# Performance work log

Hardware: AMD Instinct MI355X
Metric: run time of the kernel (lower is better)

The kernel has to match this reference:

```python
import jax, jax.numpy as jnp
import numpy as np

D_MODEL = 512
NUM_HEADS = 8
D_K = D_MODEL // NUM_HEADS
SCALE = float(np.sqrt(D_K))


def setup_inputs() -> dict:
    key = jax.random.key(0)
    ks = jax.random.split(key, 11)
    B, S, D = 2, 4096, D_MODEL
    std = 1.0 / np.sqrt(D)
    return {
        "query": jax.random.normal(ks[0], (B, S, D), jnp.float32),
        "key": jax.random.normal(ks[1], (B, S, D), jnp.float32),
        "value": jax.random.normal(ks[2], (B, S, D), jnp.float32),
        "w_q": jax.random.normal(ks[3], (D, D), jnp.float32) * std,
        "b_q": jax.random.normal(ks[4], (D,), jnp.float32) * std,
        "w_k": jax.random.normal(ks[5], (D, D), jnp.float32) * std,
        "b_k": jax.random.normal(ks[6], (D,), jnp.float32) * std,
        "w_v": jax.random.normal(ks[7], (D, D), jnp.float32) * std,
        "b_v": jax.random.normal(ks[8], (D,), jnp.float32) * std,
        "w_o": jax.random.normal(ks[9], (D, D), jnp.float32) * std,
        "b_o": jax.random.normal(ks[10], (D,), jnp.float32) * std,
    }


def reference(query, key, value, w_q, b_q, w_k, b_k, w_v, b_v, w_o, b_o):
    B, S, D = query.shape
    H, Dk = NUM_HEADS, D_K
    # Linear projections (torch Linear: x @ W^T + b), split into heads -> [B,H,S,Dk]
    Q = (query @ w_q.T + b_q).reshape(B, S, H, Dk).transpose(0, 2, 1, 3)
    K = (key @ w_k.T + b_k).reshape(B, S, H, Dk).transpose(0, 2, 1, 3)
    V = (value @ w_v.T + b_v).reshape(B, S, H, Dk).transpose(0, 2, 1, 3)
    # [B,H,S,S] attention scores — intentionally materialized like the original
    scores = jnp.einsum("bhqd,bhkd->bhqk", Q, K) / SCALE
    attn = jax.nn.softmax(scores, axis=-1)  # dropout rate 0 in eval baseline
    attended = jnp.einsum("bhqk,bhkd->bhqd", attn, V)
    attended = attended.transpose(0, 2, 1, 3).reshape(B, S, D)
    return attended @ w_o.T + b_o
```

## Files before the change

### kernel.cpp

```cpp
#include <hip/hip_runtime.h>
#include <math.h>

#define D_MODEL 512
#define NHEADS 8
#define DK 64
#define BATCH 2
#define SEQ 4096
#define NIT 32
#define ATTN_SCALE 0.18033688011112043f

typedef _Float16 half8 __attribute__((ext_vector_type(8)));
typedef _Float16 half4 __attribute__((ext_vector_type(4)));
typedef __fp16 pkhalf2 __attribute__((ext_vector_type(2)));
typedef float f32x4 __attribute__((ext_vector_type(4)));
typedef float f32x16 __attribute__((ext_vector_type(16)));

union Pk8 { _Float16 h[8]; uint4 u; };
union Pk4 { _Float16 h[4]; uint2 u; };
union Pkz { pkhalf2 h2[2]; uint2 u; };
union Un4 { uint2 u; _Float16 h[4]; };
union PFu { unsigned int u[4]; half8 h8; };

#if __has_builtin(__builtin_amdgcn_exp2f)
#define EXP2F __builtin_amdgcn_exp2f
#else
#define EXP2F exp2f
#endif

#define MFMA16(a, b, c) __builtin_amdgcn_mfma_f32_16x16x32_f16((a), (b), (c), 0, 0, 0)
#define MFMA32(a, b, c) __builtin_amdgcn_mfma_f32_32x32x16_f16((a), (b), (c), 0, 0, 0)

#define PLSWAP(x, y) asm volatile("v_permlane32_swap_b32 %0, %1" : "+v"(x), "+v"(y))

__device__ __forceinline__ unsigned int cvtpk(float a, float b) {
    union { pkhalf2 h; unsigned int u; } u_;
    u_.h = __builtin_amdgcn_cvt_pkrtz(a, b);
    return u_.u;
}

__device__ __forceinline__ void gload_lds16(const _Float16* g, _Float16* l) {
    __builtin_amdgcn_global_load_lds(
        (const __attribute__((address_space(1))) void*)g,
        (__attribute__((address_space(3))) void*)l, 16, 0, 0);
}

#define ABLK 4096
#define WBLK 256
__global__ __launch_bounds__(256)
void prep(const float* __restrict__ aq, const float* __restrict__ ak,
          const float* __restrict__ av,
          const float* __restrict__ wq, const float* __restrict__ wk,
          const float* __restrict__ wv, const float* __restrict__ wo,
          _Float16* __restrict__ dq, _Float16* __restrict__ dk,
          _Float16* __restrict__ dv,
          _Float16* __restrict__ hq, _Float16* __restrict__ hk,
          _Float16* __restrict__ hv, _Float16* __restrict__ ho) {
    int gid = blockIdx.x;
    const float* src;
    _Float16* hi;
    if (gid < 3 * ABLK) {
        const int w = gid / ABLK;
        gid -= w * ABLK;
        src = w == 0 ? aq : (w == 1 ? ak : av);
        hi  = w == 0 ? dq : (w == 1 ? dk : dv);
    } else {
        int g = gid - 3 * ABLK;
        const int w = g / WBLK;
        gid = g - w * WBLK;
        src = w == 0 ? wq : (w == 1 ? wk : (w == 2 ? wv : wo));
        hi  = w == 0 ? hq : (w == 1 ? hk : (w == 2 ? hv : ho));
    }
    const int i = (gid * 256 + threadIdx.x) * 4;
    float4 v = *(const float4*)(src + i);
    Pkz h;
    h.h2[0] = __builtin_amdgcn_cvt_pkrtz(v.x, v.y);
    h.h2[1] = __builtin_amdgcn_cvt_pkrtz(v.z, v.w);
    *(uint2*)(hi + i) = h.u;
}

__global__ __launch_bounds__(256)
void gemm_qkv(const _Float16* __restrict__ Aq, const _Float16* __restrict__ Ak,
              const _Float16* __restrict__ Av,
              const _Float16* __restrict__ Whq, const _Float16* __restrict__ Whk,
              const _Float16* __restrict__ Whv,
              const float* __restrict__ bq, const float* __restrict__ bk,
              const float* __restrict__ bv,
              _Float16* __restrict__ Qf, _Float16* __restrict__ Kf,
              _Float16* __restrict__ Vtf) {
    const int z = blockIdx.z;
    const _Float16* A    = z == 0 ? Aq  : (z == 1 ? Ak  : Av);
    const _Float16* Wh   = z == 0 ? Whq : (z == 1 ? Whk : Whv);
    const float*    bias = z == 0 ? bq  : (z == 1 ? bk  : bv);

    __shared__ __align__(16) _Float16 sA[2][128 * 64];
    __shared__ __align__(16) _Float16 sW[2][128 * 64];

    const int t    = threadIdx.x;
    const int lane = t & 63, wave = t >> 6;
    const int col  = lane & 15, quad = lane >> 4;
    const int wm   = (wave & 1) * 64, wn = (wave >> 1) * 64;
    const int m0   = blockIdx.y * 128, n0 = blockIdx.x * 128;

    const int subrow = lane >> 3;
    const int schunk = ((lane & 7) ^ subrow) * 8;

    #define STAGE_AW(K0, BUF)                                                        \
        do {                                                                          \
            _Pragma("unroll")                                                         \
            for (int j = 0; j < 4; ++j) {                                             \
                const int rw = wave * 32 + j * 8;                                     \
                gload_lds16(A  + (size_t)(m0 + rw + subrow) * 512 + (K0) + schunk,    \
                            &sA[BUF][rw * 64]);                                       \
                gload_lds16(Wh + (size_t)(n0 + rw + subrow) * 512 + (K0) + schunk,    \
                            &sW[BUF][rw * 64]);                                       \
            }                                                                         \
        } while (0)

    f32x4 acc[4][4] = {};

    STAGE_AW(0, 0);
    for (int ck = 0; ck < 8; ++ck) {
        const int cur = ck & 1;
        __syncthreads();
        if (ck + 1 < 8) STAGE_AW((ck + 1) * 64, cur ^ 1);

        #pragma unroll
        for (int kc = 0; kc < 2; ++kc) {
            const int pos = ((kc * 4 + quad) ^ (col & 7)) * 8;
            half8 af[4], wf[4];
            #pragma unroll
            for (int mt = 0; mt < 4; ++mt)
                af[mt] = *(const half8*)&sA[cur][(wm + mt * 16 + col) * 64 + pos];
            #pragma unroll
            for (int nt = 0; nt < 4; ++nt)
                wf[nt] = *(const half8*)&sW[cur][(wn + nt * 16 + col) * 64 + pos];
            #pragma unroll
            for (int mt = 0; mt < 4; ++mt)
                #pragma unroll
                for (int nt = 0; nt < 4; ++nt)
                    acc[mt][nt] = MFMA16(af[mt], wf[nt], acc[mt][nt]);
        }
    }

    float bv4[4];
    #pragma unroll
    for (int nt = 0; nt < 4; ++nt) bv4[nt] = bias[n0 + wn + nt * 16 + col];

    if (z < 2) {
        _Float16* Out = z == 0 ? Qf : Kf;
        const float alpha = z == 0 ? ATTN_SCALE : 1.0f;
        #pragma unroll
        for (int mt = 0; mt < 4; ++mt) {
            const int m = m0 + wm + mt * 16 + quad * 4;
            #pragma unroll
            for (int nt = 0; nt < 4; ++nt) {
                const int n = n0 + wn + nt * 16 + col;
                #pragma unroll
                for (int r = 0; r < 4; ++r)
                    Out[(size_t)(m + r) * 512 + n] = (_Float16)((acc[mt][nt][r] + bv4[nt]) * alpha);
            }
        }
    } else {
        #pragma unroll
        for (int mt = 0; mt < 4; ++mt) {
            const int m = m0 + wm + mt * 16 + quad * 4;
            const int b = m >> 12, s = m & (SEQ - 1);
            #pragma unroll
            for (int nt = 0; nt < 4; ++nt) {
                const int n = n0 + wn + nt * 16 + col;
                const int hh = n >> 6, d = n & (DK - 1);
                Pk4 p;
                #pragma unroll
                for (int r = 0; r < 4; ++r)
                    p.h[r] = (_Float16)(acc[mt][nt][r] + bv4[nt]);
                *(uint2*)&Vtf[((size_t)((b * NHEADS + hh) * DK + d)) * SEQ + s] = p.u;
            }
        }
    }
}

__global__ __launch_bounds__(256, 2)
void attn_mfma(const _Float16* __restrict__ Qf, const _Float16* __restrict__ Kf,
               const _Float16* __restrict__ Vtf,
               _Float16* __restrict__ Op0, _Float16* __restrict__ Op1,
               float2* __restrict__ Ml) {
    __shared__ __align__(16) _Float16 sK[2][64 * 64];
    __shared__ __align__(16) _Float16 sV[2][64 * 64];

    const int t    = threadIdx.x;
    const int lane = t & 63;
    const int wave = t >> 6;
    const int l31  = lane & 31;
    const int g    = lane >> 5;

    const int strm = blockIdx.x;
    const int h  = strm & (NHEADS - 1);
    const int z  = strm >> 3;
    const int b  = z >> 1;
    const int sp = z & 1;
    const int q0 = blockIdx.y * 256;
    const int kBase = sp * (SEQ / 2);

    const size_t rowBase = (size_t)b * SEQ;
    const size_t vBase   = ((size_t)(b * NHEADS + h)) * DK * SEQ;

    const int subrow = lane >> 3;
    const int schunk = ((lane & 7) ^ subrow) * 8;
    const _Float16* kP[2];
    const _Float16* vP[2];
    #pragma unroll
    for (int j = 0; j < 2; ++j) {
        const int rw = wave * 16 + j * 8;
        kP[j] = Kf + (rowBase + kBase + rw + subrow) * 512 + h * 64 + schunk;
        vP[j] = Vtf + vBase + (size_t)(rw + subrow) * SEQ + kBase + schunk;
        gload_lds16(kP[j], &sK[0][rw * 64]);
        gload_lds16(vP[j], &sV[0][rw * 64]);
        kP[j] += 64 * 512;
        vP[j] += 64;
    }

    half8 qf[2][4];
    #pragma unroll
    for (int qt = 0; qt < 2; ++qt)
        #pragma unroll
        for (int kc = 0; kc < 4; ++kc)
            qf[qt][kc] = *(const half8*)(Qf +
                (rowBase + q0 + wave * 64 + qt * 32 + l31) * 512 +
                h * 64 + kc * 16 + g * 8);

    const int rs = l31 & 7;

    const half8 ones = {1, 1, 1, 1, 1, 1, 1, 1};

    float m_r = 0.0f;
    f32x16 nbv = {};
    f32x16 of[2][2] = {};
    f32x16 ofl[2] = {};

    for (int itp = 0; itp < NIT; itp += 2) {
        #pragma unroll
        for (int cur = 0; cur < 2; ++cur) {
            const int it = itp + cur;
            __syncthreads();
            if (it + 1 < NIT) {
                #pragma unroll
                for (int j = 0; j < 2; ++j) {
                    const int rw = wave * 16 + j * 8;
                    gload_lds16(kP[j], &sK[cur ^ 1][rw * 64]);
                    gload_lds16(vP[j], &sV[cur ^ 1][rw * 64]);
                    kP[j] += 64 * 512;
                    vP[j] += 64;
                }
            }

            #pragma unroll
            for (int kt = 0; kt < 2; ++kt) {
                f32x16 sf0, sf1;
                __builtin_amdgcn_s_setprio(1);
                #pragma unroll
                for (int kc = 0; kc < 4; ++kc) {
                    const int pos = ((kc * 2 + g) ^ rs) * 8;
                    half8 kf = *(const half8*)&sK[cur][(kt * 32 + l31) * 64 + pos];
                    sf0 = MFMA32(kf, qf[0][kc], kc == 0 ? nbv : sf0);
                    sf1 = MFMA32(kf, qf[1][kc], kc == 0 ? nbv : sf1);
                }
                __builtin_amdgcn_s_setprio(0);

                #pragma unroll
                for (int j2 = 0; j2 < 16; ++j2) {
                    sf0[j2] = EXP2F(sf0[j2]);
                    sf1[j2] = EXP2F(sf1[j2]);
                }

                PFu pf0[2], pf1[2];
                #define MKPF(P, PF)                                                  \
                    do {                                                             \
                        unsigned int x1 = cvtpk(P[0], P[1]),  x2 = cvtpk(P[2], P[3]);\
                        unsigned int y1 = cvtpk(P[4], P[5]),  y2 = cvtpk(P[6], P[7]);\
                        PLSWAP(x1, y1); PLSWAP(x2, y2);                              \
                        PF[0].u[0] = x1; PF[0].u[1] = x2;                            \
                        PF[0].u[2] = y1; PF[0].u[3] = y2;                            \
                        unsigned int a1 = cvtpk(P[8], P[9]),  a2 = cvtpk(P[10], P[11]);\
                        unsigned int b1 = cvtpk(P[12], P[13]), b2 = cvtpk(P[14], P[15]);\
                        PLSWAP(a1, b1); PLSWAP(a2, b2);                              \
                        PF[1].u[0] = a1; PF[1].u[1] = a2;                            \
                        PF[1].u[2] = b1; PF[1].u[3] = b2;                            \
                    } while (0)
                MKPF(sf0, pf0);
                MKPF(sf1, pf1);
                #undef MKPF

                __builtin_amdgcn_s_setprio(1);
                #pragma unroll
                for (int ks2 = 0; ks2 < 2; ++ks2) {
                    const int ks = kt * 2 + ks2;
                    const int pos = ((ks * 2 + g) ^ rs) * 8;
                    half8 v0 = *(const half8*)&sV[cur][l31 * 64 + pos];
                    half8 v1 = *(const half8*)&sV[cur][(32 + l31) * 64 + pos];
                    of[0][0] = MFMA32(v0, pf0[ks2].h8, of[0][0]);
                    of[0][1] = MFMA32(v1, pf0[ks2].h8, of[0][1]);
                    of[1][0] = MFMA32(v0, pf1[ks2].h8, of[1][0]);
                    of[1][1] = MFMA32(v1, pf1[ks2].h8, of[1][1]);
                    ofl[0] = MFMA32(ones, pf0[ks2].h8, ofl[0]);
                    ofl[1] = MFMA32(ones, pf1[ks2].h8, ofl[1]);
                }
                __builtin_amdgcn_s_setprio(0);
            }

            if (__any(fmaxf(ofl[0][0], ofl[1][0]) > 1048576.0f)) {
                const float al = 0.0009765625f;
                #pragma unroll
                for (int qt = 0; qt < 2; ++qt) {
                    #pragma unroll
                    for (int j2 = 0; j2 < 16; ++j2) {
                        of[qt][0][j2] *= al;
                        of[qt][1][j2] *= al;
                        ofl[qt][j2]   *= al;
                    }
                }
                m_r += 10.0f;
                #pragma unroll
                for (int j2 = 0; j2 < 16; ++j2) nbv[j2] = -m_r;
            }
        }
    }

    _Float16* Opx = sp ? Op1 : Op0;
    #pragma unroll
    for (int qt = 0; qt < 2; ++qt) {
        const float l = ofl[qt][0];
        const float inv = 1.0f / l;
        const int q = q0 + wave * 64 + qt * 32 + l31;
        const size_t R = rowBase + q;
        #pragma unroll
        for (int dt = 0; dt < 2; ++dt) {
            #pragma unroll
            for (int m4 = 0; m4 < 4; ++m4) {
                const int d0 = dt * 32 + 8 * m4 + 4 * g;
                Pkz z2;
                z2.h2[0] = __builtin_amdgcn_cvt_pkrtz(of[qt][dt][4 * m4 + 0] * inv,
                                                      of[qt][dt][4 * m4 + 1] * inv);
                z2.h2[1] = __builtin_amdgcn_cvt_pkrtz(of[qt][dt][4 * m4 + 2] * inv,
                                                      of[qt][dt][4 * m4 + 3] * inv);
                *(uint2*)(Opx + R * 512 + h * 64 + d0) = z2.u;
            }
        }
        if (lane < 32)
            Ml[(size_t)(sp * BATCH * SEQ) * NHEADS + R * NHEADS + h] = make_float2(m_r, l);
    }
}

__global__ __launch_bounds__(256)
void attn_merge(const _Float16* __restrict__ Op0, const _Float16* __restrict__ Op1,
                const float2* __restrict__ Ml, _Float16* __restrict__ Oh) {
    const int i4 = (blockIdx.x * 256 + threadIdx.x) * 4;
    const int R = i4 >> 9;
    const int c = i4 & 511;
    const int h = c >> 6;

    const float2 ml1 = Ml[(size_t)R * NHEADS + h];
    const float2 ml2 = Ml[(size_t)(BATCH * SEQ) * NHEADS + (size_t)R * NHEADS + h];
    const float m = fmaxf(ml1.x, ml2.x);
    float w1 = EXP2F(ml1.x - m) * ml1.y;
    float w2 = EXP2F(ml2.x - m) * ml2.y;
    const float inv = 1.0f / (w1 + w2);
    w1 *= inv; w2 *= inv;

    Un4 a, bb;
    a.u  = *(const uint2*)(Op0 + (size_t)R * 512 + c);
    bb.u = *(const uint2*)(Op1 + (size_t)R * 512 + c);

    Pkz hh;
    hh.h2[0] = __builtin_amdgcn_cvt_pkrtz(w1 * (float)a.h[0] + w2 * (float)bb.h[0],
                                          w1 * (float)a.h[1] + w2 * (float)bb.h[1]);
    hh.h2[1] = __builtin_amdgcn_cvt_pkrtz(w1 * (float)a.h[2] + w2 * (float)bb.h[2],
                                          w1 * (float)a.h[3] + w2 * (float)bb.h[3]);
    *(uint2*)(Oh + (size_t)R * 512 + c) = hh.u;
}

__global__ __launch_bounds__(256)
void gemm_out(const _Float16* __restrict__ Ah, const _Float16* __restrict__ Wh,
              const float* __restrict__ bias, float* __restrict__ C) {
    __shared__ __align__(16) _Float16 sAh[2][128 * 64];
    __shared__ __align__(16) _Float16 sWh[2][64 * 64];

    const int t    = threadIdx.x;
    const int lane = t & 63, wave = t >> 6;
    const int col  = lane & 15, quad = lane >> 4;
    const int wm   = (wave & 1) * 64, wn = (wave >> 1) * 32;
    const int m0   = blockIdx.y * 128, n0 = blockIdx.x * 64;

    const int subrow = lane >> 3;
    const int schunk = ((lane & 7) ^ subrow) * 8;

    #define STAGE_OUT(K0, BUF)                                                       \
        do {                                                                          \
            _Pragma("unroll")                                                         \
            for (int j = 0; j < 4; ++j) {                                             \
                const int rw = wave * 32 + j * 8;                                     \
                gload_lds16(Ah + (size_t)(m0 + rw + subrow) * 512 + (K0) + schunk,    \
                            &sAh[BUF][rw * 64]);                                      \
            }                                                                         \
            _Pragma("unroll")                                                         \
            for (int j = 0; j < 2; ++j) {                                             \
                const int rw = wave * 16 + j * 8;                                     \
                gload_lds16(Wh + (size_t)(n0 + rw + subrow) * 512 + (K0) + schunk,    \
                            &sWh[BUF][rw * 64]);                                      \
            }                                                                         \
        } while (0)

    f32x4 acc[4][2] = {};

    STAGE_OUT(0, 0);
    for (int ck = 0; ck < 8; ++ck) {
        const int cur = ck & 1;
        __syncthreads();
        if (ck + 1 < 8) STAGE_OUT((ck + 1) * 64, cur ^ 1);

        #pragma unroll
        for (int kc = 0; kc < 2; ++kc) {
            const int pos = ((kc * 4 + quad) ^ (col & 7)) * 8;
            half8 ahf[4], whf[2];
            #pragma unroll
            for (int mt = 0; mt < 4; ++mt)
                ahf[mt] = *(const half8*)&sAh[cur][(wm + mt * 16 + col) * 64 + pos];
            #pragma unroll
            for (int nt = 0; nt < 2; ++nt)
                whf[nt] = *(const half8*)&sWh[cur][(wn + nt * 16 + col) * 64 + pos];
            #pragma unroll
            for (int mt = 0; mt < 4; ++mt)
                #pragma unroll
                for (int nt = 0; nt < 2; ++nt)
                    acc[mt][nt] = MFMA16(ahf[mt], whf[nt], acc[mt][nt]);
        }
    }

    float bv2[2];
    #pragma unroll
    for (int nt = 0; nt < 2; ++nt) bv2[nt] = bias[n0 + wn + nt * 16 + col];

    #pragma unroll
    for (int mt = 0; mt < 4; ++mt) {
        const int m = m0 + wm + mt * 16 + quad * 4;
        #pragma unroll
        for (int nt = 0; nt < 2; ++nt) {
            const int n = n0 + wn + nt * 16 + col;
            #pragma unroll
            for (int r = 0; r < 4; ++r)
                C[(size_t)(m + r) * 512 + n] = acc[mt][nt][r] + bv2[nt];
        }
    }
}

extern "C" void kernel_launch(void* const* d_in, const int* in_sizes, int n_in,
                              void* d_out, int out_size, void* d_ws, size_t ws_size,
                              hipStream_t stream) {
    const float* query = (const float*)d_in[0];
    const float* key   = (const float*)d_in[1];
    const float* value = (const float*)d_in[2];
    const float* w_q   = (const float*)d_in[3];
    const float* b_q   = (const float*)d_in[4];
    const float* w_k   = (const float*)d_in[5];
    const float* b_k   = (const float*)d_in[6];
    const float* w_v   = (const float*)d_in[7];
    const float* b_v   = (const float*)d_in[8];
    const float* w_o   = (const float*)d_in[9];
    const float* b_o   = (const float*)d_in[10];
    float* out = (float*)d_out;

    const int WN = D_MODEL * D_MODEL;
    const size_t plane = (size_t)BATCH * SEQ * D_MODEL;

    _Float16* base = (_Float16*)d_ws;
    _Float16* Aq16 = base;
    _Float16* Ak16 = Aq16 + plane;
    _Float16* Av16 = Ak16 + plane;
    _Float16* whq  = Av16 + plane;
    _Float16* whk  = whq + WN;
    _Float16* whv  = whk + WN;
    _Float16* who  = whv + WN;
    _Float16* Qf   = who + WN;
    _Float16* Kf   = Qf + plane;
    _Float16* Vtf  = Kf + plane;
    _Float16* Op1  = Vtf + plane;
    float2*   Ml   = (float2*)(Op1 + plane);
    _Float16* Oh   = Aq16;
    _Float16* Op0  = Av16;

    dim3 blk(256);

    hipLaunchKernelGGL(prep, dim3(3 * ABLK + 4 * WBLK), blk, 0, stream,
                       query, key, value, w_q, w_k, w_v, w_o,
                       Aq16, Ak16, Av16, whq, whk, whv, who);

    hipLaunchKernelGGL(gemm_qkv, dim3(D_MODEL / 128, BATCH * SEQ / 128, 3), blk, 0, stream,
                       Aq16, Ak16, Av16,
                       whq, whk, whv,
                       b_q, b_k, b_v, Qf, Kf, Vtf);

    hipLaunchKernelGGL(attn_mfma, dim3(NHEADS * BATCH * 2, SEQ / 256), blk, 0, stream,
                       Qf, Kf, Vtf, Op0, Op1, Ml);

    hipLaunchKernelGGL(attn_merge, dim3(BATCH * SEQ * D_MODEL / 4 / 256), blk, 0, stream,
                       Op0, Op1, Ml, Oh);

    hipLaunchKernelGGL(gemm_out, dim3(D_MODEL / 64, BATCH * SEQ / 128), blk, 0, stream,
                       Oh, who, b_o, out);
}
```

Before: 239.3 us.

## Split attention keys four ways and compute row sums on VALU

```diff
diff --git a/kernel.cpp b/kernel.cpp
--- a/kernel.cpp
+++ b/kernel.cpp
@@ -6,7 +6,8 @@
 #define DK 64
 #define BATCH 2
 #define SEQ 4096
-#define NIT 32
+#define NSPLIT 4
+#define NIT 16
 #define ATTN_SCALE 0.18033688011112043f
 
 typedef _Float16 half8 __attribute__((ext_vector_type(8)));
@@ -179,10 +180,11 @@
     }
 }
 
-__global__ __launch_bounds__(256, 2)
+__global__ __launch_bounds__(256, 4)
 void attn_mfma(const _Float16* __restrict__ Qf, const _Float16* __restrict__ Kf,
                const _Float16* __restrict__ Vtf,
                _Float16* __restrict__ Op0, _Float16* __restrict__ Op1,
+               _Float16* __restrict__ Op2, _Float16* __restrict__ Op3,
                float2* __restrict__ Ml) {
     __shared__ __align__(16) _Float16 sK[2][64 * 64];
     __shared__ __align__(16) _Float16 sV[2][64 * 64];
@@ -196,10 +198,10 @@
     const int strm = blockIdx.x;
     const int h  = strm & (NHEADS - 1);
     const int z  = strm >> 3;
-    const int b  = z >> 1;
-    const int sp = z & 1;
+    const int b  = z >> 2;
+    const int sp = z & 3;
     const int q0 = blockIdx.y * 256;
-    const int kBase = sp * (SEQ / 2);
+    const int kBase = sp * (SEQ / NSPLIT);
 
     const size_t rowBase = (size_t)b * SEQ;
     const size_t vBase   = ((size_t)(b * NHEADS + h)) * DK * SEQ;
@@ -230,12 +232,10 @@
 
     const int rs = l31 & 7;
 
-    const half8 ones = {1, 1, 1, 1, 1, 1, 1, 1};
-
     float m_r = 0.0f;
     f32x16 nbv = {};
+    float l_r[2] = { 0.0f, 0.0f };
     f32x16 of[2][2] = {};
-    f32x16 ofl[2] = {};
 
     for (int itp = 0; itp < NIT; itp += 2) {
         #pragma unroll
@@ -266,11 +266,14 @@
                 }
                 __builtin_amdgcn_s_setprio(0);
 
+                float lrs0 = 0.0f, lrs1 = 0.0f;
                 #pragma unroll
                 for (int j2 = 0; j2 < 16; ++j2) {
-                    sf0[j2] = EXP2F(sf0[j2]);
-                    sf1[j2] = EXP2F(sf1[j2]);
+                    sf0[j2] = EXP2F(sf0[j2]);  lrs0 += sf0[j2];
+                    sf1[j2] = EXP2F(sf1[j2]);  lrs1 += sf1[j2];
                 }
+                l_r[0] += lrs0;
+                l_r[1] += lrs1;
 
                 PFu pf0[2], pf1[2];
                 #define MKPF(P, PF)                                                  \
@@ -301,21 +304,19 @@
                     of[0][1] = MFMA32(v1, pf0[ks2].h8, of[0][1]);
                     of[1][0] = MFMA32(v0, pf1[ks2].h8, of[1][0]);
                     of[1][1] = MFMA32(v1, pf1[ks2].h8, of[1][1]);
-                    ofl[0] = MFMA32(ones, pf0[ks2].h8, ofl[0]);
-                    ofl[1] = MFMA32(ones, pf1[ks2].h8, ofl[1]);
                 }
                 __builtin_amdgcn_s_setprio(0);
             }
 
-            if (__any(fmaxf(ofl[0][0], ofl[1][0]) > 1048576.0f)) {
+            if (__any(fmaxf(l_r[0], l_r[1]) > 1048576.0f)) {
                 const float al = 0.0009765625f;
                 #pragma unroll
                 for (int qt = 0; qt < 2; ++qt) {
+                    l_r[qt] *= al;
                     #pragma unroll
                     for (int j2 = 0; j2 < 16; ++j2) {
                         of[qt][0][j2] *= al;
                         of[qt][1][j2] *= al;
-                        ofl[qt][j2]   *= al;
                     }
                 }
                 m_r += 10.0f;
@@ -325,10 +326,10 @@
         }
     }
 
-    _Float16* Opx = sp ? Op1 : Op0;
+    _Float16* Opx = sp == 0 ? Op0 : (sp == 1 ? Op1 : (sp == 2 ? Op2 : Op3));
     #pragma unroll
     for (int qt = 0; qt < 2; ++qt) {
-        const float l = ofl[qt][0];
+        const float l = l_r[qt] + __shfl_xor(l_r[qt], 32);
         const float inv = 1.0f / l;
         const int q = q0 + wave * 64 + qt * 32 + l31;
         const size_t R = rowBase + q;
@@ -346,35 +347,47 @@
             }
         }
         if (lane < 32)
-            Ml[(size_t)(sp * BATCH * SEQ) * NHEADS + R * NHEADS + h] = make_float2(m_r, l);
+            Ml[((size_t)sp * BATCH * SEQ + R) * NHEADS + h] = make_float2(m_r, l);
     }
 }
 
 __global__ __launch_bounds__(256)
 void attn_merge(const _Float16* __restrict__ Op0, const _Float16* __restrict__ Op1,
+                const _Float16* __restrict__ Op2, const _Float16* __restrict__ Op3,
                 const float2* __restrict__ Ml, _Float16* __restrict__ Oh) {
     const int i4 = (blockIdx.x * 256 + threadIdx.x) * 4;
     const int R = i4 >> 9;
     const int c = i4 & 511;
     const int h = c >> 6;
 
-    const float2 ml1 = Ml[(size_t)R * NHEADS + h];
-    const float2 ml2 = Ml[(size_t)(BATCH * SEQ) * NHEADS + (size_t)R * NHEADS + h];
-    const float m = fmaxf(ml1.x, ml2.x);
+    const size_t mlStride = (size_t)BATCH * SEQ * NHEADS;
+    const size_t mlIdx = (size_t)R * NHEADS + h;
+    float2 ml0 = Ml[mlIdx];
+    float2 ml1 = Ml[mlStride + mlIdx];
+    float2 ml2 = Ml[2 * mlStride + mlIdx];
+    float2 ml3 = Ml[3 * mlStride + mlIdx];
+    const float m = fmaxf(fmaxf(ml0.x, ml1.x), fmaxf(ml2.x, ml3.x));
+    float w0 = EXP2F(ml0.x - m) * ml0.y;
     float w1 = EXP2F(ml1.x - m) * ml1.y;
     float w2 = EXP2F(ml2.x - m) * ml2.y;
-    const float inv = 1.0f / (w1 + w2);
-    w1 *= inv; w2 *= inv;
-
-    Un4 a, bb;
+    float w3 = EXP2F(ml3.x - m) * ml3.y;
+    const float inv = 1.0f / (w0 + w1 + w2 + w3);
+    w0 *= inv; w1 *= inv; w2 *= inv; w3 *= inv;
+
+    Un4 a, bb, cc, dd;
     a.u  = *(const uint2*)(Op0 + (size_t)R * 512 + c);
     bb.u = *(const uint2*)(Op1 + (size_t)R * 512 + c);
+    cc.u = *(const uint2*)(Op2 + (size_t)R * 512 + c);
+    dd.u = *(const uint2*)(Op3 + (size_t)R * 512 + c);
+
+    float o0 = w0 * (float)a.h[0] + w1 * (float)bb.h[0] + w2 * (float)cc.h[0] + w3 * (float)dd.h[0];
+    float o1 = w0 * (float)a.h[1] + w1 * (float)bb.h[1] + w2 * (float)cc.h[1] + w3 * (float)dd.h[1];
+    float o2 = w0 * (float)a.h[2] + w1 * (float)bb.h[2] + w2 * (float)cc.h[2] + w3 * (float)dd.h[2];
+    float o3 = w0 * (float)a.h[3] + w1 * (float)bb.h[3] + w2 * (float)cc.h[3] + w3 * (float)dd.h[3];
 
     Pkz hh;
-    hh.h2[0] = __builtin_amdgcn_cvt_pkrtz(w1 * (float)a.h[0] + w2 * (float)bb.h[0],
-                                          w1 * (float)a.h[1] + w2 * (float)bb.h[1]);
-    hh.h2[1] = __builtin_amdgcn_cvt_pkrtz(w1 * (float)a.h[2] + w2 * (float)bb.h[2],
-                                          w1 * (float)a.h[3] + w2 * (float)bb.h[3]);
+    hh.h2[0] = __builtin_amdgcn_cvt_pkrtz(o0, o1);
+    hh.h2[1] = __builtin_amdgcn_cvt_pkrtz(o2, o3);
     *(uint2*)(Oh + (size_t)R * 512 + c) = hh.u;
 }
 
@@ -486,6 +499,8 @@
     float2*   Ml   = (float2*)(Op1 + plane);
     _Float16* Oh   = Aq16;
     _Float16* Op0  = Av16;
+    _Float16* Op2  = Ak16;
+    _Float16* Op3  = Aq16;
 
     dim3 blk(256);
 
@@ -498,11 +513,11 @@
                        whq, whk, whv,
                        b_q, b_k, b_v, Qf, Kf, Vtf);
 
-    hipLaunchKernelGGL(attn_mfma, dim3(NHEADS * BATCH * 2, SEQ / 256), blk, 0, stream,
-                       Qf, Kf, Vtf, Op0, Op1, Ml);
+    hipLaunchKernelGGL(attn_mfma, dim3(NHEADS * BATCH * NSPLIT, SEQ / 256), blk, 0, stream,
+                       Qf, Kf, Vtf, Op0, Op1, Op2, Op3, Ml);
 
     hipLaunchKernelGGL(attn_merge, dim3(BATCH * SEQ * D_MODEL / 4 / 256), blk, 0, stream,
-                       Op0, Op1, Ml, Oh);
+                       Op0, Op1, Op2, Op3, Ml, Oh);
 
     hipLaunchKernelGGL(gemm_out, dim3(D_MODEL / 64, BATCH * SEQ / 128), blk, 0, stream,
                        Oh, who, b_o, out);
```

After: 880.5 us. +268.0%, slower.

## Fuse activation fp16 conversion into QKV GEMM and compute softmax sums on VALU

Applied to the files above, without the earlier changes.

```diff
diff --git a/kernel.cpp b/kernel.cpp
--- a/kernel.cpp
+++ b/kernel.cpp
@@ -6,6 +6,7 @@
 #define DK 64
 #define BATCH 2
 #define SEQ 4096
+#define NSPLIT 2
 #define NIT 32
 #define ATTN_SCALE 0.18033688011112043f
 
@@ -44,32 +45,17 @@
         (__attribute__((address_space(3))) void*)l, 16, 0, 0);
 }
 
-#define ABLK 4096
 #define WBLK 256
 __global__ __launch_bounds__(256)
-void prep(const float* __restrict__ aq, const float* __restrict__ ak,
-          const float* __restrict__ av,
-          const float* __restrict__ wq, const float* __restrict__ wk,
+void prep(const float* __restrict__ wq, const float* __restrict__ wk,
           const float* __restrict__ wv, const float* __restrict__ wo,
-          _Float16* __restrict__ dq, _Float16* __restrict__ dk,
-          _Float16* __restrict__ dv,
           _Float16* __restrict__ hq, _Float16* __restrict__ hk,
           _Float16* __restrict__ hv, _Float16* __restrict__ ho) {
     int gid = blockIdx.x;
-    const float* src;
-    _Float16* hi;
-    if (gid < 3 * ABLK) {
-        const int w = gid / ABLK;
-        gid -= w * ABLK;
-        src = w == 0 ? aq : (w == 1 ? ak : av);
-        hi  = w == 0 ? dq : (w == 1 ? dk : dv);
-    } else {
-        int g = gid - 3 * ABLK;
-        const int w = g / WBLK;
-        gid = g - w * WBLK;
-        src = w == 0 ? wq : (w == 1 ? wk : (w == 2 ? wv : wo));
-        hi  = w == 0 ? hq : (w == 1 ? hk : (w == 2 ? hv : ho));
-    }
+    const int w = gid / WBLK;
+    gid -= w * WBLK;
+    const float* src = w == 0 ? wq : (w == 1 ? wk : (w == 2 ? wv : wo));
+    _Float16* hi     = w == 0 ? hq : (w == 1 ? hk : (w == 2 ? hv : ho));
     const int i = (gid * 256 + threadIdx.x) * 4;
     float4 v = *(const float4*)(src + i);
     Pkz h;
@@ -79,8 +65,8 @@
 }
 
 __global__ __launch_bounds__(256)
-void gemm_qkv(const _Float16* __restrict__ Aq, const _Float16* __restrict__ Ak,
-              const _Float16* __restrict__ Av,
+void gemm_qkv(const float* __restrict__ Aq, const float* __restrict__ Ak,
+              const float* __restrict__ Av,
               const _Float16* __restrict__ Whq, const _Float16* __restrict__ Whk,
               const _Float16* __restrict__ Whv,
               const float* __restrict__ bq, const float* __restrict__ bk,
@@ -88,7 +74,7 @@
               _Float16* __restrict__ Qf, _Float16* __restrict__ Kf,
               _Float16* __restrict__ Vtf) {
     const int z = blockIdx.z;
-    const _Float16* A    = z == 0 ? Aq  : (z == 1 ? Ak  : Av);
+    const float*    A    = z == 0 ? Aq  : (z == 1 ? Ak  : Av);
     const _Float16* Wh   = z == 0 ? Whq : (z == 1 ? Whk : Whv);
     const float*    bias = z == 0 ? bq  : (z == 1 ? bk  : bv);
 
@@ -104,25 +90,53 @@
     const int subrow = lane >> 3;
     const int schunk = ((lane & 7) ^ subrow) * 8;
 
-    #define STAGE_AW(K0, BUF)                                                        \
-        do {                                                                          \
-            _Pragma("unroll")                                                         \
-            for (int j = 0; j < 4; ++j) {                                             \
-                const int rw = wave * 32 + j * 8;                                     \
-                gload_lds16(A  + (size_t)(m0 + rw + subrow) * 512 + (K0) + schunk,    \
-                            &sA[BUF][rw * 64]);                                       \
-                gload_lds16(Wh + (size_t)(n0 + rw + subrow) * 512 + (K0) + schunk,    \
-                            &sW[BUF][rw * 64]);                                       \
-            }                                                                         \
+    const float* aBase = A + (size_t)(m0 + wave * 32 + subrow) * 512 + schunk;
+
+    float4 ar[4][2];
+    #define LOAD_A(K0)                                                            \
+        do {                                                                       \
+            _Pragma("unroll")                                                      \
+            for (int j = 0; j < 4; ++j) {                                          \
+                const float* s = aBase + (size_t)(j * 8) * 512 + (K0);             \
+                ar[j][0] = *(const float4*)s;                                      \
+                ar[j][1] = *(const float4*)(s + 4);                                \
+            }                                                                      \
         } while (0)
+    #define WRITE_A(BUF)                                                           \
+        do {                                                                       \
+            _Pragma("unroll")                                                      \
+            for (int j = 0; j < 4; ++j) {                                          \
+                uint4 p;                                                           \
+                p.x = cvtpk(ar[j][0].x, ar[j][0].y);                               \
+                p.y = cvtpk(ar[j][0].z, ar[j][0].w);                               \
+                p.z = cvtpk(ar[j][1].x, ar[j][1].y);                               \
+                p.w = cvtpk(ar[j][1].z, ar[j][1].w);                               \
+                *(uint4*)&sA[BUF][(wave * 32 + j * 8) * 64 + lane * 8] = p;        \
+            }                                                                      \
+        } while (0)
+    #define STAGE_W(K0, BUF)                                                       \
+        do {                                                                       \
+            _Pragma("unroll")                                                      \
+            for (int j = 0; j < 4; ++j) {                                          \
+                const int rw = wave * 32 + j * 8;                                  \
+                gload_lds16(Wh + (size_t)(n0 + rw + subrow) * 512 + (K0) + schunk, \
+                            &sW[BUF][rw * 64]);                                    \
+            }                                                                      \
+        } while (0)
 
     f32x4 acc[4][4] = {};
 
-    STAGE_AW(0, 0);
+    STAGE_W(0, 0);
+    LOAD_A(0);
+    WRITE_A(0);
+
     for (int ck = 0; ck < 8; ++ck) {
         const int cur = ck & 1;
         __syncthreads();
-        if (ck + 1 < 8) STAGE_AW((ck + 1) * 64, cur ^ 1);
+        if (ck + 1 < 8) {
+            STAGE_W((ck + 1) * 64, cur ^ 1);
+            LOAD_A((ck + 1) * 64);
+        }
 
         #pragma unroll
         for (int kc = 0; kc < 2; ++kc) {
@@ -140,6 +154,8 @@
                 for (int nt = 0; nt < 4; ++nt)
                     acc[mt][nt] = MFMA16(af[mt], wf[nt], acc[mt][nt]);
         }
+
+        if (ck + 1 < 8) WRITE_A(cur ^ 1);
     }
 
     float bv4[4];
@@ -199,7 +215,7 @@
     const int b  = z >> 1;
     const int sp = z & 1;
     const int q0 = blockIdx.y * 256;
-    const int kBase = sp * (SEQ / 2);
+    const int kBase = sp * (SEQ / NSPLIT);
 
     const size_t rowBase = (size_t)b * SEQ;
     const size_t vBase   = ((size_t)(b * NHEADS + h)) * DK * SEQ;
@@ -230,12 +246,10 @@
 
     const int rs = l31 & 7;
 
-    const half8 ones = {1, 1, 1, 1, 1, 1, 1, 1};
-
     float m_r = 0.0f;
     f32x16 nbv = {};
+    float l_r[2] = { 0.0f, 0.0f };
     f32x16 of[2][2] = {};
-    f32x16 ofl[2] = {};
 
     for (int itp = 0; itp < NIT; itp += 2) {
         #pragma unroll
@@ -266,11 +280,14 @@
                 }
                 __builtin_amdgcn_s_setprio(0);
 
+                float lrs0 = 0.0f, lrs1 = 0.0f;
                 #pragma unroll
                 for (int j2 = 0; j2 < 16; ++j2) {
-                    sf0[j2] = EXP2F(sf0[j2]);
-                    sf1[j2] = EXP2F(sf1[j2]);
+                    sf0[j2] = EXP2F(sf0[j2]);  lrs0 += sf0[j2];
+                    sf1[j2] = EXP2F(sf1[j2]);  lrs1 += sf1[j2];
                 }
+                l_r[0] += lrs0;
+                l_r[1] += lrs1;
 
                 PFu pf0[2], pf1[2];
                 #define MKPF(P, PF)                                                  \
@@ -301,21 +318,19 @@
                     of[0][1] = MFMA32(v1, pf0[ks2].h8, of[0][1]);
                     of[1][0] = MFMA32(v0, pf1[ks2].h8, of[1][0]);
                     of[1][1] = MFMA32(v1, pf1[ks2].h8, of[1][1]);
-                    ofl[0] = MFMA32(ones, pf0[ks2].h8, ofl[0]);
-                    ofl[1] = MFMA32(ones, pf1[ks2].h8, ofl[1]);
                 }
                 __builtin_amdgcn_s_setprio(0);
             }
 
-            if (__any(fmaxf(ofl[0][0], ofl[1][0]) > 1048576.0f)) {
+            if (__any(fmaxf(l_r[0], l_r[1]) > 1048576.0f)) {
                 const float al = 0.0009765625f;
                 #pragma unroll
                 for (int qt = 0; qt < 2; ++qt) {
+                    l_r[qt] *= al;
                     #pragma unroll
                     for (int j2 = 0; j2 < 16; ++j2) {
                         of[qt][0][j2] *= al;
                         of[qt][1][j2] *= al;
-                        ofl[qt][j2]   *= al;
                     }
                 }
                 m_r += 10.0f;
@@ -328,7 +343,7 @@
     _Float16* Opx = sp ? Op1 : Op0;
     #pragma unroll
     for (int qt = 0; qt < 2; ++qt) {
-        const float l = ofl[qt][0];
+        const float l = l_r[qt] + __shfl_xor(l_r[qt], 32);
         const float inv = 1.0f / l;
         const int q = q0 + wave * 64 + qt * 32 + l31;
         const size_t R = rowBase + q;
@@ -346,7 +361,7 @@
             }
         }
         if (lane < 32)
-            Ml[(size_t)(sp * BATCH * SEQ) * NHEADS + R * NHEADS + h] = make_float2(m_r, l);
+            Ml[((size_t)sp * BATCH * SEQ + R) * NHEADS + h] = make_float2(m_r, l);
     }
 }
 
@@ -489,16 +504,15 @@
 
     dim3 blk(256);
 
-    hipLaunchKernelGGL(prep, dim3(3 * ABLK + 4 * WBLK), blk, 0, stream,
-                       query, key, value, w_q, w_k, w_v, w_o,
-                       Aq16, Ak16, Av16, whq, whk, whv, who);
+    hipLaunchKernelGGL(prep, dim3(4 * WBLK), blk, 0, stream,
+                       w_q, w_k, w_v, w_o, whq, whk, whv, who);
 
     hipLaunchKernelGGL(gemm_qkv, dim3(D_MODEL / 128, BATCH * SEQ / 128, 3), blk, 0, stream,
-                       Aq16, Ak16, Av16,
+                       query, key, value,
                        whq, whk, whv,
                        b_q, b_k, b_v, Qf, Kf, Vtf);
 
-    hipLaunchKernelGGL(attn_mfma, dim3(NHEADS * BATCH * 2, SEQ / 256), blk, 0, stream,
+    hipLaunchKernelGGL(attn_mfma, dim3(NHEADS * BATCH * NSPLIT, SEQ / 256), blk, 0, stream,
                        Qf, Kf, Vtf, Op0, Op1, Ml);
 
     hipLaunchKernelGGL(attn_merge, dim3(BATCH * SEQ * D_MODEL / 4 / 256), blk, 0, stream,
```

Measured after the change: 240.1 us. No clear change (+0.3%).
